# Kernel optimization log

Measured on AMD Instinct MI355X. Metric: run time of the kernel, lower is better.

The kernel has to match this reference:

```python
import jax, jax.numpy as jnp
import numpy as np
from jax import lax

LEAK = 0.01   # nn.LeakyReLU default negative slope
EPS = 1e-5    # BatchNorm2d eps


def _conv(x, w, b, stride, pad):
    # torch Conv2d, NCHW / OIHW
    y = lax.conv_general_dilated(x, w, (stride, stride), [(pad, pad), (pad, pad)],
                                 dimension_numbers=('NCHW', 'OIHW', 'NCHW'))
    return y + b[None, :, None, None]


def _bn_lrelu(x, g, b):
    # BatchNorm2d in training mode (torch default): batch statistics over (N,H,W)
    m = jnp.mean(x, axis=(0, 2, 3), keepdims=True)
    v = jnp.var(x, axis=(0, 2, 3), keepdims=True)
    xn = (x - m) * lax.rsqrt(v + EPS) * g[None, :, None, None] + b[None, :, None, None]
    return jnp.where(xn >= 0, xn, LEAK * xn)


def _convt(x, w, b):
    # ConvTranspose2d with stride == kernel_size, padding=0: non-overlapping
    # k x k expansion of every pixel -> expressible as one einsum + reshape.
    # w: (Cin, Cout, k, k) (torch ConvTranspose2d layout)
    B, C, H, W = x.shape
    _, Co, k, _ = w.shape
    y = jnp.einsum('bchw,coij->bohiwj', x, w).reshape(B, Co, H * k, W * k)
    return y + b[None, :, None, None]


def setup_inputs() -> dict:
    key = jax.random.key(0)
    ks = iter(jax.random.split(key, 64))
    def rn(shape, s=0.05):
        return jax.random.normal(next(ks), shape, dtype=jnp.float32) * s
    d = {}
    d['x'] = jax.random.normal(next(ks), (16, 3, 128, 128), dtype=jnp.float32)
    enc_shapes = [(64, 3, 4, 4), (128, 64, 4, 4), (256, 128, 4, 4), (256, 256, 4, 4)]
    for i, s in enumerate(enc_shapes):
        d[f'enc_w{i}'] = rn(s)
        d[f'enc_b{i}'] = jnp.zeros((s[0],), jnp.float32)
    for i, c in enumerate([64, 128, 256]):
        d[f'ebn_g{i}'] = jnp.ones((c,), jnp.float32)
        d[f'ebn_b{i}'] = jnp.zeros((c,), jnp.float32)
    d['codebook'] = rn((512, 256), 1.0)  # (codebook_size, latent_dim)
    dec_shapes = [(256, 128, 4, 4), (128, 64, 2, 2), (64, 32, 2, 2)]
    for i, s in enumerate(dec_shapes):
        d[f'dec_w{i}'] = rn(s)
        d[f'dec_b{i}'] = jnp.zeros((s[1],), jnp.float32)
        d[f'dbn_g{i}'] = jnp.ones((s[1],), jnp.float32)
        d[f'dbn_b{i}'] = jnp.zeros((s[1],), jnp.float32)
    d['dec_w3'] = rn((3, 32, 1, 1))
    d['dec_b3'] = jnp.zeros((3,), jnp.float32)
    return d


def reference(x,
              enc_w0, enc_b0, ebn_g0, ebn_b0,
              enc_w1, enc_b1, ebn_g1, ebn_b1,
              enc_w2, enc_b2, ebn_g2, ebn_b2,
              enc_w3, enc_b3,
              codebook,
              dec_w0, dec_b0, dbn_g0, dbn_b0,
              dec_w1, dec_b1, dbn_g1, dbn_b1,
              dec_w2, dec_b2, dbn_g2, dbn_b2,
              dec_w3, dec_b3):
    # ---- encoder ----
    h = _bn_lrelu(_conv(x, enc_w0, enc_b0, 2, 1), ebn_g0, ebn_b0)   # (B,64,64,64)
    h = _bn_lrelu(_conv(h, enc_w1, enc_b1, 2, 1), ebn_g1, ebn_b1)   # (B,128,32,32)
    h = _bn_lrelu(_conv(h, enc_w2, enc_b2, 2, 1), ebn_g2, ebn_b2)   # (B,256,16,16)
    z = _conv(h, enc_w3, enc_b3, 2, 1)                               # (B,256,8,8)

    # ---- vector quantizer ----
    B, C, H, W = z.shape
    zf = z.transpose(0, 2, 3, 1).reshape(-1, C)                      # (BHW, C)
    # squared L2 distances to every codebook entry
    d2 = (jnp.sum(zf * zf, axis=-1, keepdims=True)
          - 2.0 * zf @ codebook.T
          + jnp.sum(codebook * codebook, axis=-1)[None, :])          # (BHW, K)
    idx = jnp.argmin(d2, axis=-1)                                    # (BHW,)
    min_d = jnp.min(d2, axis=-1)
    q = codebook[idx]                                                # (BHW, C)
    commitment_loss = jnp.mean((lax.stop_gradient(q) - zf) ** 2)
    codebook_loss = jnp.mean((q - lax.stop_gradient(zf)) ** 2)
    q_st = zf + lax.stop_gradient(q - zf)                            # straight-through
    qz = q_st.reshape(B, H, W, C).transpose(0, 3, 1, 2)              # (B,256,8,8)

    # ---- decoder ----
    h = _bn_lrelu(_convt(qz, dec_w0, dec_b0), dbn_g0, dbn_b0)        # (B,128,32,32)
    h = _bn_lrelu(_convt(h, dec_w1, dec_b1), dbn_g1, dbn_b1)         # (B,64,64,64)
    h = _bn_lrelu(_convt(h, dec_w2, dec_b2), dbn_g2, dbn_b2)         # (B,32,128,128)
    out = jnp.tanh(jnp.einsum('bchw,oc->bohw', h, dec_w3[:, :, 0, 0])
                   + dec_b3[None, :, None, None])                    # (B,3,128,128)

    return (out, commitment_loss, codebook_loss,
            idx.reshape(B, H, W), min_d.reshape(B, H, W))
```

## Files before the change

kernel.cpp:

```cpp
#include <hip/hip_runtime.h>
#include <math.h>

#define LEAK 0.01f

typedef __bf16 bf16x8 __attribute__((ext_vector_type(8)));
typedef float f32x4 __attribute__((ext_vector_type(4)));
typedef unsigned short ushort;
typedef unsigned int uint32;

struct HL { ushort h, l; };

__device__ inline HL split_bf16(float x) {
    unsigned u = __float_as_uint(x);
    unsigned hr = (u + 0x7FFFu + ((u >> 16) & 1u)) >> 16;
    float fh = __uint_as_float(hr << 16);
    float r = x - fh;
    unsigned v = __float_as_uint(r);
    unsigned lr = (v + 0x7FFFu + ((v >> 16) & 1u)) >> 16;
    HL out; out.h = (ushort)hr; out.l = (ushort)lr;
    return out;
}

template<int MODE>
__device__ inline void stage_load(float (&pv)[2][4], const float* __restrict__ Bf,
                                  int kbase, int n0, int tid,
                                  int Ci, int Hin, int Ho, int lgHo, int lgHW) {
#pragma unroll
    for (int r = 0; r < 2; ++r) {
        int g = r * 256 + tid;
        int nl = g >> 3, kg = g & 7;
        int n = n0 + nl;
        if (MODE == 0) {
            int k4 = kbase + (kg << 2);
            int ic = k4 >> 4, kh = (k4 >> 2) & 3;
            int ow = n & (Ho - 1), oh = (n >> lgHo) & (Ho - 1), b = n >> (lgHo + lgHo);
            int ih = oh * 2 - 1 + kh;
            int ihc = ih < 0 ? 0 : (ih >= Hin ? Hin - 1 : ih);
            int iwb = ow * 2 - 1;
            size_t base = ((size_t)(b * Ci + ic) * Hin + ihc) * Hin;
#pragma unroll
            for (int e = 0; e < 4; ++e) {
                int iw = iwb + e;
                int iwc = iw < 0 ? 0 : (iw >= Hin ? Hin - 1 : iw);
                pv[r][e] = Bf[base + iwc];
            }
        } else {
            int c = kbase + (kg << 2);
            int b = n >> lgHW, hw = n & ((1 << lgHW) - 1);
            size_t base = (((size_t)(b * Ci + c)) << lgHW) + hw;
            size_t str = (size_t)1 << lgHW;
#pragma unroll
            for (int e = 0; e < 4; ++e) pv[r][e] = Bf[base + e * str];
        }
    }
}

template<int MODE>
__global__ __launch_bounds__(256, 3) void gemm_mfma(
    const ushort* __restrict__ Ah, const ushort* __restrict__ Al,
    const float* __restrict__ Bf,
    const float* __restrict__ bnt, const float* __restrict__ gamma,
    const float* __restrict__ beta, float invN, int chanShift,
    const float* __restrict__ bias, float* __restrict__ P,
    int Mtiles, int Ntiles, int K, int Kslice, int KS, int outSize,
    int Ci, int Hin, int Co, int Ho, int lgHo,
    int lgHW, int lgHin, int lgCo, int lgk,
    float* __restrict__ statsBnt, const float* __restrict__ bnPart)
{
    __shared__ __align__(16) uint32 Bsp[64 * 36];
    __shared__ float scs[256], shs[256];

    int bid = blockIdx.x;
    int ntile = bid % Ntiles; bid /= Ntiles;
    int mtile = bid % Mtiles;
    int ks = bid / Mtiles;
    int tid = threadIdx.x;
    int lane = tid & 63, w = tid >> 6;
    int quad = lane >> 4, tl = lane & 15;
    int n0 = ntile << 6, m0 = mtile << 7, k0 = ks * Kslice;
    int Kt = K >> 5;

    bool useBN = (bnt != nullptr) || (bnPart != nullptr);
    int c0 = k0 >> chanShift;
    if (bnPart != nullptr) {
        int c = tid >> 2, qq = tid & 3;
        const float2* pp2 = (const float2*)(bnPart + c * 512) + qq * 64;
        float s = 0.f, s2 = 0.f;
#pragma unroll 8
        for (int p = 0; p < 64; ++p) { float2 v = pp2[p]; s += v.x; s2 += v.y; }
        scs[tid] = s; shs[tid] = s2;
        __syncthreads();
        float scale = 0.f, shift = 0.f;
        if (tid < 64) {
            float st = scs[tid * 4] + scs[tid * 4 + 1] + scs[tid * 4 + 2] + scs[tid * 4 + 3];
            float qt = shs[tid * 4] + shs[tid * 4 + 1] + shs[tid * 4 + 2] + shs[tid * 4 + 3];
            float m = st * invN;
            float var = qt * invN - m * m;
            scale = gamma[tid] * rsqrtf(var + 1e-5f);
            shift = beta[tid] - m * scale;
        }
        __syncthreads();
        if (tid < 64 && tid >= c0) { scs[tid - c0] = scale; shs[tid - c0] = shift; }
    } else if (bnt != nullptr) {
        int nch = Kslice >> chanShift;
        for (int c = tid; c < nch; c += 256) {
            float m = bnt[(c0 + c) * 2] * invN;
            float var = bnt[(c0 + c) * 2 + 1] * invN - m * m;
            float scale = gamma[c0 + c] * rsqrtf(var + 1e-5f);
            scs[c] = scale;
            shs[c] = beta[c0 + c] - m * scale;
        }
    }
    __syncthreads();

    f32x4 zero4 = {0.f, 0.f, 0.f, 0.f};
    f32x4 acc[2][4];
#pragma unroll
    for (int mt = 0; mt < 2; ++mt)
#pragma unroll
        for (int nt = 0; nt < 4; ++nt) acc[mt][nt] = zero4;

    float pv[2][4];
    stage_load<MODE>(pv, Bf, k0, n0, tid, Ci, Hin, Ho, lgHo, lgHW);

    for (int kc = 0; kc < Kslice; kc += 32) {
        int kbase = k0 + kc;
        int kt = kbase >> 5;
#pragma unroll
        for (int r = 0; r < 2; ++r) {
            int g = r * 256 + tid;
            int nl = g >> 3, kg = g & 7;
            int k4 = kbase + (kg << 2);
            uint32 pk[4];
            if (MODE == 0) {
                int ic = k4 >> 4, kh = (k4 >> 2) & 3;
                int n = n0 + nl;
                int ow = n & (Ho - 1), oh = (n >> lgHo) & (Ho - 1);
                int ih = oh * 2 - 1 + kh;
                bool rowok = (unsigned)ih < (unsigned)Hin;
                int iwb = ow * 2 - 1;
                float sc_ = useBN ? scs[ic - c0] : 0.f;
                float sh_ = useBN ? shs[ic - c0] : 0.f;
#pragma unroll
                for (int e = 0; e < 4; ++e) {
                    int iw = iwb + e;
                    bool ok = rowok && ((unsigned)iw < (unsigned)Hin);
                    float f = pv[r][e];
                    if (useBN) { f = f * sc_ + sh_; f = f >= 0.f ? f : LEAK * f; }
                    if (!ok) f = 0.f;
                    HL s = split_bf16(f);
                    pk[e] = ((uint32)s.h << 16) | s.l;
                }
            } else {
#pragma unroll
                for (int e = 0; e < 4; ++e) {
                    float f = pv[r][e];
                    if (useBN) {
                        int lc = k4 + e - k0;
                        f = f * scs[lc] + shs[lc];
                        f = f >= 0.f ? f : LEAK * f;
                    }
                    HL s = split_bf16(f);
                    pk[e] = ((uint32)s.h << 16) | s.l;
                }
            }
            *(uint4*)&Bsp[nl * 36 + (kg << 2)] = make_uint4(pk[0], pk[1], pk[2], pk[3]);
        }
        __syncthreads();

        bool more = (kc + 32) < Kslice;
        float pvn[2][4];
        if (more) stage_load<MODE>(pvn, Bf, kbase + 32, n0, tid, Ci, Hin, Ho, lgHo, lgHW);

        bf16x8 afh[2], afl[2];
#pragma unroll
        for (int mt = 0; mt < 2; ++mt) {
            int mtAbs = (m0 >> 4) + (w << 1) + mt;
            size_t abase = (((size_t)mtAbs * Kt + kt) << 6) + lane;
            afh[mt] = *(const bf16x8*)(Ah + abase * 8);
            afl[mt] = *(const bf16x8*)(Al + abase * 8);
        }
        bf16x8 bfh[4], bfl[4];
#pragma unroll
        for (int nt = 0; nt < 4; ++nt) {
            int base = ((nt << 4) + tl) * 36 + (quad << 3);
            uint4 ua = *(const uint4*)&Bsp[base];
            uint4 ub = *(const uint4*)&Bsp[base + 4];
            union { uint32 u[4]; bf16x8 v; } H, L;
            H.u[0] = __builtin_amdgcn_perm(ua.y, ua.x, 0x07060302u);
            H.u[1] = __builtin_amdgcn_perm(ua.w, ua.z, 0x07060302u);
            H.u[2] = __builtin_amdgcn_perm(ub.y, ub.x, 0x07060302u);
            H.u[3] = __builtin_amdgcn_perm(ub.w, ub.z, 0x07060302u);
            L.u[0] = __builtin_amdgcn_perm(ua.y, ua.x, 0x05040100u);
            L.u[1] = __builtin_amdgcn_perm(ua.w, ua.z, 0x05040100u);
            L.u[2] = __builtin_amdgcn_perm(ub.y, ub.x, 0x05040100u);
            L.u[3] = __builtin_amdgcn_perm(ub.w, ub.z, 0x05040100u);
            bfh[nt] = H.v; bfl[nt] = L.v;
        }
#pragma unroll
        for (int mt = 0; mt < 2; ++mt)
#pragma unroll
            for (int nt = 0; nt < 4; ++nt) {
                acc[mt][nt] = __builtin_amdgcn_mfma_f32_16x16x32_bf16(afh[mt], bfh[nt], acc[mt][nt], 0, 0, 0);
                acc[mt][nt] = __builtin_amdgcn_mfma_f32_16x16x32_bf16(afh[mt], bfl[nt], acc[mt][nt], 0, 0, 0);
                acc[mt][nt] = __builtin_amdgcn_mfma_f32_16x16x32_bf16(afl[mt], bfh[nt], acc[mt][nt], 0, 0, 0);
            }
        __syncthreads();
        if (more) {
#pragma unroll
            for (int r = 0; r < 2; ++r)
#pragma unroll
                for (int e = 0; e < 4; ++e) pv[r][e] = pvn[r][e];
        }
    }

    bool doStats = (statsBnt != nullptr);
    if (doStats) {
        if (tid < 2 * Co) scs[tid] = 0.f;
        __syncthreads();
    }
    float ssum[2][4] = {{0.f,0.f,0.f,0.f},{0.f,0.f,0.f,0.f}};
    float ssq [2][4] = {{0.f,0.f,0.f,0.f},{0.f,0.f,0.f,0.f}};
    float* dst = P + (size_t)ks * outSize;
    if (MODE == 0) {
#pragma unroll
        for (int nt = 0; nt < 4; ++nt) {
            int n = n0 + (nt << 4) + tl;
            int ow = n & (Ho - 1), oh = (n >> lgHo) & (Ho - 1), b = n >> (lgHo + lgHo);
#pragma unroll
            for (int mt = 0; mt < 2; ++mt) {
                int mb = m0 + (w << 5) + (mt << 4) + (quad << 2);
#pragma unroll
                for (int r = 0; r < 4; ++r) {
                    int oc = mb + r;
                    float v = acc[mt][nt][r];
                    if (KS == 1) v += bias[oc];
                    if (doStats) { ssum[mt][r] += v; ssq[mt][r] += v * v; }
                    dst[((size_t)(b * Co + oc) * Ho + oh) * Ho + ow] = v;
                }
            }
        }
    } else {
        int kf = 1 << lgk;
        int Ho2 = Hin << lgk;
#pragma unroll
        for (int nt = 0; nt < 4; ++nt) {
            int n = n0 + (nt << 4) + tl;
            int b = n >> lgHW, hw = n & ((1 << lgHW) - 1);
            int h = hw >> lgHin, wp = hw & (Hin - 1);
#pragma unroll
            for (int mt = 0; mt < 2; ++mt) {
                int mb = m0 + (w << 5) + (mt << 4) + (quad << 2);
#pragma unroll
                for (int r = 0; r < 4; ++r) {
                    int m = mb + r;
                    int o = m & (Co - 1), ij = m >> lgCo;
                    int ii = ij >> lgk, jj = ij & (kf - 1);
                    float v = acc[mt][nt][r];
                    if (KS == 1) v += bias[o];
                    if (doStats) { ssum[mt][r] += v; ssq[mt][r] += v * v; }
                    dst[((size_t)(b * Co + o) * Ho2 + (h << lgk) + ii) * Ho2 + (wp << lgk) + jj] = v;
                }
            }
        }
    }
    if (doStats) {
#pragma unroll
        for (int mt = 0; mt < 2; ++mt)
#pragma unroll
            for (int r = 0; r < 4; ++r) {
                float s = ssum[mt][r], q2 = ssq[mt][r];
#pragma unroll
                for (int m2 = 1; m2 < 16; m2 <<= 1) {
                    s  += __shfl_xor(s,  m2);
                    q2 += __shfl_xor(q2, m2);
                }
                if (tl == 0) {
                    int m = m0 + (w << 5) + (mt << 4) + (quad << 2) + r;
                    int o = (MODE == 0) ? m : (m & (Co - 1));
                    atomicAdd(&scs[o * 2],     s);
                    atomicAdd(&scs[o * 2 + 1], q2);
                }
            }
        __syncthreads();
        if (tid < 2 * Co) atomicAdd(&statsBnt[tid], scs[tid]);
    }
}

__device__ inline int fragaddr(int m, int k, int K) {
    return ((((m >> 4) * (K >> 5) + (k >> 5)) << 9) | (((k >> 3) & 3) << 7) | ((m & 15) << 3) | (k & 7));
}

#define OUT_CL   786432
#define OUT_CB   786433
#define OUT_IDX  786434
#define OUT_MIND 787458

__device__ void conv_body(int bid, int tid,
                          const float* __restrict__ x, const float* __restrict__ w,
                          const float* __restrict__ bias, float* __restrict__ P,
                          float* __restrict__ pst, float (&cst)[4][16])
{
    const int Ci = 3, Hin = 128, Co = 64, Ho = 64, OCT = 8;
    int ntile = (16 * Ho * Ho) >> 8;
    int tile = bid % ntile;
    int og = bid / ntile;
    int oc0 = og * OCT;

    int px = (tile << 8) + tid;
    int ow = px % Ho; int t = px / Ho;
    int oh = t % Ho;  int b = t / Ho;

    int off[16]; float fm[16];
    int ih0 = oh * 2 - 1, iw0 = ow * 2 - 1;
#pragma unroll
    for (int kh = 0; kh < 4; ++kh)
#pragma unroll
        for (int kw = 0; kw < 4; ++kw) {
            int ih = ih0 + kh, iw = iw0 + kw;
            bool ok = (ih >= 0) && (ih < Hin) && (iw >= 0) && (iw < Hin);
            int ihc = ih < 0 ? 0 : (ih >= Hin ? Hin - 1 : ih);
            int iwc = iw < 0 ? 0 : (iw >= Hin ? Hin - 1 : iw);
            off[kh * 4 + kw] = ihc * Hin + iwc;
            fm[kh * 4 + kw] = ok ? 1.f : 0.f;
        }

    float acc[OCT];
#pragma unroll
    for (int u = 0; u < OCT; ++u) acc[u] = bias[oc0 + u];

    const float* xc = x + (size_t)b * Ci * Hin * Hin;
    const float* wi = w + (size_t)oc0 * Ci * 16;
    int HinHin = Hin * Hin;
    for (int ic = 0; ic < Ci; ++ic) {
        float xv[16];
#pragma unroll
        for (int q = 0; q < 16; ++q) xv[q] = xc[off[q]] * fm[q];
#pragma unroll
        for (int u = 0; u < OCT; ++u) {
            const float* wo = wi + (size_t)u * Ci * 16;
            float a = acc[u];
#pragma unroll
            for (int q = 0; q < 16; ++q) a += xv[q] * wo[q];
            acc[u] = a;
        }
        xc += HinHin;
        wi += 16;
    }
    size_t obase = (((size_t)b * Co + oc0) * Ho + oh) * Ho + ow;
    size_t opl = (size_t)Ho * Ho;
#pragma unroll
    for (int u = 0; u < OCT; ++u) P[obase + u * opl] = acc[u];

    float sv[OCT], qv[OCT];
#pragma unroll
    for (int u = 0; u < OCT; ++u) { sv[u] = acc[u]; qv[u] = acc[u] * acc[u]; }
#pragma unroll
    for (int m2 = 1; m2 < 64; m2 <<= 1)
#pragma unroll
        for (int u = 0; u < OCT; ++u) {
            sv[u] += __shfl_xor(sv[u], m2);
            qv[u] += __shfl_xor(qv[u], m2);
        }
    int lane = tid & 63, wv = tid >> 6;
    if (lane == 0) {
#pragma unroll
        for (int u = 0; u < OCT; ++u) { cst[wv][u * 2] = sv[u]; cst[wv][u * 2 + 1] = qv[u]; }
    }
    __syncthreads();
    if (tid < 2 * OCT) {
        float v = cst[0][tid] + cst[1][tid] + cst[2][tid] + cst[3][tid];
        pst[(oc0 + (tid >> 1)) * 512 + tile * 2 + (tid & 1)] = v;
    }
}

__global__ void prologue(const float* __restrict__ w1, const float* __restrict__ w2,
                         const float* __restrict__ w3, const float* __restrict__ d0,
                         const float* __restrict__ d1, const float* __restrict__ d2,
                         ushort* __restrict__ WH, ushort* __restrict__ WL,
                         const float* __restrict__ cb, float* __restrict__ cbT,
                         float* __restrict__ bnt, float* __restrict__ dout,
                         const float* __restrict__ x, const float* __restrict__ w0,
                         const float* __restrict__ b0, float* __restrict__ Y0,
                         float* __restrict__ pst) {
    __shared__ float cst[4][16];
    int blk = blockIdx.x;
    int tid = threadIdx.x;
    if (blk < 24) {
        bnt[blk * 256 + tid] = 0.f;
        if (blk == 0 && tid < 2) dout[OUT_CL + tid] = 0.f;
        return;
    }
    if (blk < 536) {
        int idx = (blk - 24) * 256 + tid;
        int k = idx & 511, c = idx >> 9;
        cbT[idx] = cb[k * 256 + c];
        return;
    }
    if (blk >= 9400) {
        conv_body(blk - 9400, tid, x, w0, b0, Y0, pst, cst);
        return;
    }
    int idx = (blk - 536) * 256 + tid;
    if (idx >= 2269184) return;
    float v; int dst;
    if (idx < 131072) {
        int m = idx >> 10, k = idx & 1023;
        v = w1[idx];
        dst = fragaddr(m, k, 1024);
    } else if (idx < 655360) {
        int i = idx - 131072;
        int m = i >> 11, k = i & 2047;
        v = w2[i];
        dst = 131072 + fragaddr(m, k, 2048);
    } else if (idx < 1703936) {
        int i = idx - 655360;
        int m = i >> 12, k = i & 4095;
        v = w3[i];
        dst = 655360 + fragaddr(m, k, 4096);
    } else if (idx < 2228224) {
        int i = idx - 1703936;
        int m = i >> 8, c = i & 255;
        int o = m & 127, ij = m >> 7;
        v = d0[((size_t)c * 128 + o) * 16 + ij];
        dst = 1703936 + fragaddr(m, c, 256);
    } else if (idx < 2260992) {
        int i = idx - 2228224;
        int m = i >> 7, c = i & 127;
        int o = m & 63, ij = m >> 6;
        v = d1[((size_t)c * 64 + o) * 4 + ij];
        dst = 2228224 + fragaddr(m, c, 128);
    } else {
        int i = idx - 2260992;
        int m = i >> 6, c = i & 63;
        int o = m & 31, ij = m >> 5;
        v = d2[((size_t)c * 32 + o) * 4 + ij];
        dst = 2260992 + fragaddr(m, c, 64);
    }
    HL s = split_bf16(v);
    WH[dst] = s.h; WL[dst] = s.l;
}

__global__ void reduce_bias_stats4(const float4* __restrict__ P, const float* __restrict__ bias,
                                   float4* __restrict__ y, float* __restrict__ bnt,
                                   int outSize4, int KS, int Co, int HW4, int nch) {
    int tid = threadIdx.x;
    int i = blockIdx.x * 256 + tid;
    int c = (i / HW4) % Co;
    float bv = bias[c];
    float4 s = make_float4(bv, bv, bv, bv);
    for (int ks = 0; ks < KS; ++ks) {
        float4 p = P[(size_t)ks * outSize4 + i];
        s.x += p.x; s.y += p.y; s.z += p.z; s.w += p.w;
    }
    y[i] = s;
    float ls  = s.x + s.y + s.z + s.w;
    float ls2 = s.x * s.x + s.y * s.y + s.z * s.z + s.w * s.w;
    __shared__ float as[16], aq[16];
    if (tid < 16) { as[tid] = 0.f; aq[tid] = 0.f; }
    __syncthreads();
    int c0 = ((blockIdx.x * 256) / HW4) % Co;
    atomicAdd(&as[c - c0], ls);
    atomicAdd(&aq[c - c0], ls2);
    __syncthreads();
    if (tid < nch) {
        atomicAdd(&bnt[(c0 + tid) * 2],     as[tid]);
        atomicAdd(&bnt[(c0 + tid) * 2 + 1], aq[tid]);
    }
}

__global__ void vq_main(const float* __restrict__ Pz, const float* __restrict__ b3,
                        const float* __restrict__ cbT, const float* __restrict__ cb,
                        float* __restrict__ q, float* __restrict__ dout) {
    int r0 = blockIdx.x * 4;
    int tid = threadIdx.x;
    int lane = tid & 63, w = tid >> 6;

    __shared__ __align__(16) float zT[256][4];
    __shared__ float wred[4][4];
    __shared__ float zn2s[4];
    __shared__ float wbd[4][4];
    __shared__ int   wbi[4][4];
    __shared__ int   bestsh[4];
    __shared__ float bestd[4];

    int b = r0 >> 6, s0 = r0 & 63;
    size_t zi = ((size_t)(b * 256 + tid)) * 64 + s0;
    float bv = b3[tid];
    float4 zv = make_float4(bv, bv, bv, bv);
    const float4* pp = (const float4*)Pz + (zi >> 2);
#pragma unroll
    for (int ks = 0; ks < 16; ++ks) {
        float4 p = pp[(size_t)ks * 65536];
        zv.x += p.x; zv.y += p.y; zv.z += p.z; zv.w += p.w;
    }
    *(float4*)&zT[tid][0] = zv;

    float p0 = zv.x * zv.x, p1 = zv.y * zv.y, p2 = zv.z * zv.z, p3 = zv.w * zv.w;
#pragma unroll
    for (int m2 = 1; m2 < 64; m2 <<= 1) {
        p0 += __shfl_xor(p0, m2); p1 += __shfl_xor(p1, m2);
        p2 += __shfl_xor(p2, m2); p3 += __shfl_xor(p3, m2);
    }
    if (lane == 0) { wred[w][0] = p0; wred[w][1] = p1; wred[w][2] = p2; wred[w][3] = p3; }
    __syncthreads();
    if (tid < 4) zn2s[tid] = wred[0][tid] + wred[1][tid] + wred[2][tid] + wred[3][tid];
    __syncthreads();

    float d0[4], d1[4];
#pragma unroll
    for (int rr = 0; rr < 4; ++rr) { d0[rr] = 0.f; d1[rr] = 0.f; }
    float cn0 = 0.f, cn1 = 0.f;
#pragma unroll 4
    for (int c = 0; c < 256; ++c) {
        float cv0 = cbT[c * 512 + tid];
        float cv1 = cbT[c * 512 + 256 + tid];
        cn0 += cv0 * cv0;
        cn1 += cv1 * cv1;
        float4 za = *(const float4*)&zT[c][0];
        d0[0] += za.x * cv0; d1[0] += za.x * cv1;
        d0[1] += za.y * cv0; d1[1] += za.y * cv1;
        d0[2] += za.z * cv0; d1[2] += za.z * cv1;
        d0[3] += za.w * cv0; d1[3] += za.w * cv1;
    }

#pragma unroll
    for (int rr = 0; rr < 4; ++rr) {
        float dist0 = zn2s[rr] - 2.f * d0[rr] + cn0;
        float dist1 = zn2s[rr] - 2.f * d1[rr] + cn1;
        float bd = dist0; int bi = tid;
        if (dist1 < bd) { bd = dist1; bi = tid + 256; }
#pragma unroll
        for (int m2 = 1; m2 < 64; m2 <<= 1) {
            float od = __shfl_xor(bd, m2); int oi = __shfl_xor(bi, m2);
            if (od < bd || (od == bd && oi < bi)) { bd = od; bi = oi; }
        }
        if (lane == 0) { wbd[w][rr] = bd; wbi[w][rr] = bi; }
    }
    __syncthreads();
    if (tid < 4) {
        float bd = wbd[0][tid]; int bi = wbi[0][tid];
#pragma unroll
        for (int ww = 1; ww < 4; ++ww) {
            float od = wbd[ww][tid]; int oi = wbi[ww][tid];
            if (od < bd || (od == bd && oi < bi)) { bd = od; bi = oi; }
        }
        bestsh[tid] = bi; bestd[tid] = bd;
        dout[OUT_IDX + r0 + tid]  = (float)bi;
        dout[OUT_MIND + r0 + tid] = bd;
    }
    __syncthreads();

    float4 qv;
    qv.x = cb[(size_t)bestsh[0] * 256 + tid];
    qv.y = cb[(size_t)bestsh[1] * 256 + tid];
    qv.z = cb[(size_t)bestsh[2] * 256 + tid];
    qv.w = cb[(size_t)bestsh[3] * 256 + tid];
    *(float4*)&q[((size_t)(b * 256 + tid)) * 64 + s0] = qv;
    if (tid == 0) {
        float ls = (bestd[0] + bestd[1] + bestd[2] + bestd[3]) * (1.f / 262144.f);
        atomicAdd(&dout[OUT_CL], ls);
        atomicAdd(&dout[OUT_CB], ls);
    }
}

__global__ void final_conv_tanh(const float* __restrict__ hbuf, const float* __restrict__ bnt,
                                const float* __restrict__ g, const float* __restrict__ bt,
                                const float* __restrict__ w3, const float* __restrict__ b3,
                                float* __restrict__ out) {
    __shared__ float sc[32], sh[32], sw[96];
    int tid = threadIdx.x;
    if (tid < 32) {
        float m = bnt[tid * 2] * (1.f / 262144.f);
        float var = bnt[tid * 2 + 1] * (1.f / 262144.f) - m * m;
        float scale = g[tid] * rsqrtf(var + 1e-5f);
        sc[tid] = scale;
        sh[tid] = bt[tid] - m * scale;
    }
    if (tid < 96) sw[tid] = w3[tid];
    __syncthreads();
    int idx = blockIdx.x * 256 + tid;
    int hw4 = idx & 4095;
    int b   = idx >> 12;
    const float4* hp = (const float4*)hbuf + ((size_t)b * 32) * 4096 + hw4;
    float b0 = b3[0], b1 = b3[1], b2 = b3[2];
    float4 a0 = make_float4(b0, b0, b0, b0);
    float4 a1 = make_float4(b1, b1, b1, b1);
    float4 a2 = make_float4(b2, b2, b2, b2);
#pragma unroll 8
    for (int c = 0; c < 32; ++c) {
        float4 v = hp[(size_t)c * 4096];
        float scv = sc[c], shv = sh[c];
        float vx = v.x * scv + shv; vx = vx >= 0.f ? vx : LEAK * vx;
        float vy = v.y * scv + shv; vy = vy >= 0.f ? vy : LEAK * vy;
        float vz = v.z * scv + shv; vz = vz >= 0.f ? vz : LEAK * vz;
        float vw = v.w * scv + shv; vw = vw >= 0.f ? vw : LEAK * vw;
        float w0 = sw[c], w1 = sw[32 + c], w2 = sw[64 + c];
        a0.x += vx * w0; a0.y += vy * w0; a0.z += vz * w0; a0.w += vw * w0;
        a1.x += vx * w1; a1.y += vy * w1; a1.z += vz * w1; a1.w += vw * w1;
        a2.x += vx * w2; a2.y += vy * w2; a2.z += vz * w2; a2.w += vw * w2;
    }
    float4* op = (float4*)out;
    size_t ob = ((size_t)b * 3) * 4096 + hw4;
    op[ob]            = make_float4(tanhf(a0.x), tanhf(a0.y), tanhf(a0.z), tanhf(a0.w));
    op[ob + 4096]     = make_float4(tanhf(a1.x), tanhf(a1.y), tanhf(a1.z), tanhf(a1.w));
    op[ob + 2 * 4096] = make_float4(tanhf(a2.x), tanhf(a2.y), tanhf(a2.z), tanhf(a2.w));
}

extern "C" void kernel_launch(void* const* d_in, const int* in_sizes, int n_in,
                              void* d_out, int out_size, void* d_ws, size_t ws_size,
                              hipStream_t stream) {
    const float* x      = (const float*)d_in[0];
    const float* enc_w0 = (const float*)d_in[1];
    const float* enc_b0 = (const float*)d_in[2];
    const float* enc_w1 = (const float*)d_in[3];
    const float* enc_b1 = (const float*)d_in[4];
    const float* enc_w2 = (const float*)d_in[5];
    const float* enc_b2 = (const float*)d_in[6];
    const float* enc_w3 = (const float*)d_in[7];
    const float* enc_b3 = (const float*)d_in[8];
    const float* ebn_g0 = (const float*)d_in[9];
    const float* ebn_b0 = (const float*)d_in[10];
    const float* ebn_g1 = (const float*)d_in[11];
    const float* ebn_b1 = (const float*)d_in[12];
    const float* ebn_g2 = (const float*)d_in[13];
    const float* ebn_b2 = (const float*)d_in[14];
    const float* cb     = (const float*)d_in[15];
    const float* dec_w0 = (const float*)d_in[16];
    const float* dec_b0 = (const float*)d_in[17];
    const float* dbn_g0 = (const float*)d_in[18];
    const float* dbn_b0 = (const float*)d_in[19];
    const float* dec_w1 = (const float*)d_in[20];
    const float* dec_b1 = (const float*)d_in[21];
    const float* dbn_g1 = (const float*)d_in[22];
    const float* dbn_b1 = (const float*)d_in[23];
    const float* dec_w2 = (const float*)d_in[24];
    const float* dec_b2 = (const float*)d_in[25];
    const float* dbn_g2 = (const float*)d_in[26];
    const float* dbn_b2 = (const float*)d_in[27];
    const float* dec_w3 = (const float*)d_in[28];
    const float* dec_b3 = (const float*)d_in[29];

    float* out = (float*)d_out;
    float* ws  = (float*)d_ws;

    float*  Y0   = ws;
    float*  Y1   = ws + 4194304;
    float*  Y2   = ws + 6291456;
    float*  PST  = ws + 7340032;
    float*  Q    = ws + 7602176;
    ushort* WH   = (ushort*)(ws + 7864320);
    ushort* WL   = (ushort*)(ws + 8998912);
    float*  CBT  = ws + 10133504;
    float*  BNT  = ws + 10264576;
    float*  PART = ws + 10270720;
    float*  D0   = ws + 18659328;
    float*  D1   = ws + 20756480;
    float*  D2   = ws + 24950784;

    dim3 blk(256);

    prologue<<<11448, blk, 0, stream>>>(enc_w1, enc_w2, enc_w3, dec_w0, dec_w1, dec_w2,
                                        WH, WL, cb, CBT, BNT, out,
                                        x, enc_w0, enc_b0, Y0, PST);

    gemm_mfma<0><<<512, blk, 0, stream>>>(WH, WL, Y0,
        nullptr, ebn_g0, ebn_b0, 1.f / 65536.f, 4, enc_b1, PART,
        1, 256, 1024, 512, 2, 2097152, 64, 64, 128, 32, 5, 0, 0, 0, 0, nullptr, PST);
    reduce_bias_stats4<<<2048, blk, 0, stream>>>((const float4*)PART, enc_b1, (float4*)Y1,
                                                 BNT + 1024, 524288, 2, 128, 256, 1);

    gemm_mfma<0><<<512, blk, 0, stream>>>(WH + 131072, WL + 131072, Y1,
        BNT + 1024, ebn_g1, ebn_b1, 1.f / 16384.f, 4, enc_b2, PART,
        2, 64, 2048, 512, 4, 1048576, 128, 32, 256, 16, 4, 0, 0, 0, 0, nullptr, nullptr);
    reduce_bias_stats4<<<1024, blk, 0, stream>>>((const float4*)PART, enc_b2, (float4*)Y2,
                                                 BNT + 2048, 262144, 4, 256, 64, 4);

    gemm_mfma<0><<<512, blk, 0, stream>>>(WH + 655360, WL + 655360, Y2,
        BNT + 2048, ebn_g2, ebn_b2, 1.f / 4096.f, 4, enc_b3, PART,
        2, 16, 4096, 256, 16, 262144, 256, 16, 256, 8, 3, 0, 0, 0, 0, nullptr, nullptr);

    vq_main<<<256, blk, 0, stream>>>(PART, enc_b3, CBT, cb, Q, out);

    gemm_mfma<1><<<512, blk, 0, stream>>>(WH + 1703936, WL + 1703936, Q,
        nullptr, nullptr, nullptr, 0.f, 0, dec_b0, PART,
        16, 16, 256, 128, 2, 2097152, 256, 8, 128, 0, 0, 6, 3, 7, 2, nullptr, nullptr);
    reduce_bias_stats4<<<2048, blk, 0, stream>>>((const float4*)PART, dec_b0, (float4*)D0,
                                                 BNT + 3072, 524288, 2, 128, 256, 1);

    gemm_mfma<1><<<512, blk, 0, stream>>>(WH + 2228224, WL + 2228224, D0,
        BNT + 3072, dbn_g0, dbn_b0, 1.f / 16384.f, 0, dec_b1, D1,
        2, 256, 128, 128, 1, 0, 128, 32, 64, 0, 0, 10, 5, 6, 1, BNT + 4096, nullptr);

    gemm_mfma<1><<<1024, blk, 0, stream>>>(WH + 2260992, WL + 2260992, D1,
        BNT + 4096, dbn_g1, dbn_b1, 1.f / 65536.f, 0, dec_b2, D2,
        1, 1024, 64, 64, 1, 0, 64, 64, 32, 0, 0, 12, 6, 5, 1, BNT + 5120, nullptr);

    final_conv_tanh<<<256, blk, 0, stream>>>(D2, BNT + 5120, dbn_g2, dbn_b2, dec_w3, dec_b3, out);
}
```

Measured before the change: 416.9 us.

## Emit pre-split bf16 quantized latents and bank BN stat atomics across eight slots

The VQ kernel now writes the quantized vectors as pre-split bf16 hi/lo arrays in row-major (pixel, channel) layout. A new GEMM mode 2 loads these directly as MFMA B fragments from global memory, skipping LDS staging, the split conversion and the block barriers for the first decoder layer. Separately, per-block BN statistic atomics are spread over eight banks indexed by block id, and consumers sum the banks, to reduce atomic contention. The risks are that direct global fragment loads may coalesce poorly, and that the bank buffers need zero-initialisation that is not shown here.

```diff
diff --git a/kernel.cpp b/kernel.cpp
--- a/kernel.cpp
+++ b/kernel.cpp
@@ -65,7 +65,8 @@
     int Mtiles, int Ntiles, int K, int Kslice, int KS, int outSize,
     int Ci, int Hin, int Co, int Ho, int lgHo,
     int lgHW, int lgHin, int lgCo, int lgk,
-    float* __restrict__ statsBnt, const float* __restrict__ bnPart)
+    float* __restrict__ statsBnt, const float* __restrict__ bnPart,
+    int statsBank, int bntBankStride)
 {
     __shared__ __align__(16) uint32 Bsp[64 * 36];
     __shared__ float scs[256], shs[256];
@@ -104,8 +105,20 @@
     } else if (bnt != nullptr) {
         int nch = Kslice >> chanShift;
         for (int c = tid; c < nch; c += 256) {
-            float m = bnt[(c0 + c) * 2] * invN;
-            float var = bnt[(c0 + c) * 2 + 1] * invN - m * m;
+            float sm, sq;
+            if (bntBankStride > 0) {
+                sm = 0.f; sq = 0.f;
+#pragma unroll
+                for (int bk = 0; bk < 8; ++bk) {
+                    sm += bnt[bk * bntBankStride + (c0 + c) * 2];
+                    sq += bnt[bk * bntBankStride + (c0 + c) * 2 + 1];
+                }
+            } else {
+                sm = bnt[(c0 + c) * 2];
+                sq = bnt[(c0 + c) * 2 + 1];
+            }
+            float m = sm * invN;
+            float var = sq * invN - m * m;
             float scale = gamma[c0 + c] * rsqrtf(var + 1e-5f);
             scs[c] = scale;
             shs[c] = beta[c0 + c] - m * scale;
@@ -121,56 +134,58 @@
         for (int nt = 0; nt < 4; ++nt) acc[mt][nt] = zero4;
 
     float pv[2][4];
-    stage_load<MODE>(pv, Bf, k0, n0, tid, Ci, Hin, Ho, lgHo, lgHW);
+    if (MODE != 2) stage_load<MODE>(pv, Bf, k0, n0, tid, Ci, Hin, Ho, lgHo, lgHW);
 
     for (int kc = 0; kc < Kslice; kc += 32) {
         int kbase = k0 + kc;
         int kt = kbase >> 5;
-#pragma unroll
-        for (int r = 0; r < 2; ++r) {
-            int g = r * 256 + tid;
-            int nl = g >> 3, kg = g & 7;
-            int k4 = kbase + (kg << 2);
-            uint32 pk[4];
-            if (MODE == 0) {
-                int ic = k4 >> 4, kh = (k4 >> 2) & 3;
-                int n = n0 + nl;
-                int ow = n & (Ho - 1), oh = (n >> lgHo) & (Ho - 1);
-                int ih = oh * 2 - 1 + kh;
-                bool rowok = (unsigned)ih < (unsigned)Hin;
-                int iwb = ow * 2 - 1;
-                float sc_ = useBN ? scs[ic - c0] : 0.f;
-                float sh_ = useBN ? shs[ic - c0] : 0.f;
-#pragma unroll
-                for (int e = 0; e < 4; ++e) {
-                    int iw = iwb + e;
-                    bool ok = rowok && ((unsigned)iw < (unsigned)Hin);
-                    float f = pv[r][e];
-                    if (useBN) { f = f * sc_ + sh_; f = f >= 0.f ? f : LEAK * f; }
-                    if (!ok) f = 0.f;
-                    HL s = split_bf16(f);
-                    pk[e] = ((uint32)s.h << 16) | s.l;
-                }
-            } else {
-#pragma unroll
-                for (int e = 0; e < 4; ++e) {
-                    float f = pv[r][e];
-                    if (useBN) {
-                        int lc = k4 + e - k0;
-                        f = f * scs[lc] + shs[lc];
-                        f = f >= 0.f ? f : LEAK * f;
-                    }
-                    HL s = split_bf16(f);
-                    pk[e] = ((uint32)s.h << 16) | s.l;
-                }
-            }
-            *(uint4*)&Bsp[nl * 36 + (kg << 2)] = make_uint4(pk[0], pk[1], pk[2], pk[3]);
-        }
-        __syncthreads();
-
         bool more = (kc + 32) < Kslice;
         float pvn[2][4];
-        if (more) stage_load<MODE>(pvn, Bf, kbase + 32, n0, tid, Ci, Hin, Ho, lgHo, lgHW);
+        if (MODE != 2) {
+#pragma unroll
+            for (int r = 0; r < 2; ++r) {
+                int g = r * 256 + tid;
+                int nl = g >> 3, kg = g & 7;
+                int k4 = kbase + (kg << 2);
+                uint32 pk[4];
+                if (MODE == 0) {
+                    int ic = k4 >> 4, kh = (k4 >> 2) & 3;
+                    int n = n0 + nl;
+                    int ow = n & (Ho - 1), oh = (n >> lgHo) & (Ho - 1);
+                    int ih = oh * 2 - 1 + kh;
+                    bool rowok = (unsigned)ih < (unsigned)Hin;
+                    int iwb = ow * 2 - 1;
+                    float sc_ = useBN ? scs[ic - c0] : 0.f;
+                    float sh_ = useBN ? shs[ic - c0] : 0.f;
+#pragma unroll
+                    for (int e = 0; e < 4; ++e) {
+                        int iw = iwb + e;
+                        bool ok = rowok && ((unsigned)iw < (unsigned)Hin);
+                        float f = pv[r][e];
+                        if (useBN) { f = f * sc_ + sh_; f = f >= 0.f ? f : LEAK * f; }
+                        if (!ok) f = 0.f;
+                        HL s = split_bf16(f);
+                        pk[e] = ((uint32)s.h << 16) | s.l;
+                    }
+                } else {
+#pragma unroll
+                    for (int e = 0; e < 4; ++e) {
+                        float f = pv[r][e];
+                        if (useBN) {
+                            int lc = k4 + e - k0;
+                            f = f * scs[lc] + shs[lc];
+                            f = f >= 0.f ? f : LEAK * f;
+                        }
+                        HL s = split_bf16(f);
+                        pk[e] = ((uint32)s.h << 16) | s.l;
+                    }
+                }
+                *(uint4*)&Bsp[nl * 36 + (kg << 2)] = make_uint4(pk[0], pk[1], pk[2], pk[3]);
+            }
+            __syncthreads();
+
+            if (more) stage_load<MODE>(pvn, Bf, kbase + 32, n0, tid, Ci, Hin, Ho, lgHo, lgHW);
+        }
 
         bf16x8 afh[2], afl[2];
 #pragma unroll
@@ -181,21 +196,32 @@
             afl[mt] = *(const bf16x8*)(Al + abase * 8);
         }
         bf16x8 bfh[4], bfl[4];
-#pragma unroll
-        for (int nt = 0; nt < 4; ++nt) {
-            int base = ((nt << 4) + tl) * 36 + (quad << 3);
-            uint4 ua = *(const uint4*)&Bsp[base];
-            uint4 ub = *(const uint4*)&Bsp[base + 4];
-            union { uint32 u[4]; bf16x8 v; } H, L;
-            H.u[0] = __builtin_amdgcn_perm(ua.y, ua.x, 0x07060302u);
-            H.u[1] = __builtin_amdgcn_perm(ua.w, ua.z, 0x07060302u);
-            H.u[2] = __builtin_amdgcn_perm(ub.y, ub.x, 0x07060302u);
-            H.u[3] = __builtin_amdgcn_perm(ub.w, ub.z, 0x07060302u);
-            L.u[0] = __builtin_amdgcn_perm(ua.y, ua.x, 0x05040100u);
-            L.u[1] = __builtin_amdgcn_perm(ua.w, ua.z, 0x05040100u);
-            L.u[2] = __builtin_amdgcn_perm(ub.y, ub.x, 0x05040100u);
-            L.u[3] = __builtin_amdgcn_perm(ub.w, ub.z, 0x05040100u);
-            bfh[nt] = H.v; bfl[nt] = L.v;
+        if (MODE == 2) {
+            const ushort* Bu = (const ushort*)Bf;
+#pragma unroll
+            for (int nt = 0; nt < 4; ++nt) {
+                int n = n0 + (nt << 4) + tl;
+                size_t ba = (size_t)n * Ci + kbase + (quad << 3);
+                bfh[nt] = *(const bf16x8*)(Bu + ba);
+                bfl[nt] = *(const bf16x8*)(Bu + Ho + ba);
+            }
+        } else {
+#pragma unroll
+            for (int nt = 0; nt < 4; ++nt) {
+                int base = ((nt << 4) + tl) * 36 + (quad << 3);
+                uint4 ua = *(const uint4*)&Bsp[base];
+                uint4 ub = *(const uint4*)&Bsp[base + 4];
+                union { uint32 u[4]; bf16x8 v; } H, L;
+                H.u[0] = __builtin_amdgcn_perm(ua.y, ua.x, 0x07060302u);
+                H.u[1] = __builtin_amdgcn_perm(ua.w, ua.z, 0x07060302u);
+                H.u[2] = __builtin_amdgcn_perm(ub.y, ub.x, 0x07060302u);
+                H.u[3] = __builtin_amdgcn_perm(ub.w, ub.z, 0x07060302u);
+                L.u[0] = __builtin_amdgcn_perm(ua.y, ua.x, 0x05040100u);
+                L.u[1] = __builtin_amdgcn_perm(ua.w, ua.z, 0x05040100u);
+                L.u[2] = __builtin_amdgcn_perm(ub.y, ub.x, 0x05040100u);
+                L.u[3] = __builtin_amdgcn_perm(ub.w, ub.z, 0x05040100u);
+                bfh[nt] = H.v; bfl[nt] = L.v;
+            }
         }
 #pragma unroll
         for (int mt = 0; mt < 2; ++mt)
@@ -205,12 +231,14 @@
                 acc[mt][nt] = __builtin_amdgcn_mfma_f32_16x16x32_bf16(afh[mt], bfl[nt], acc[mt][nt], 0, 0, 0);
                 acc[mt][nt] = __builtin_amdgcn_mfma_f32_16x16x32_bf16(afl[mt], bfh[nt], acc[mt][nt], 0, 0, 0);
             }
-        __syncthreads();
-        if (more) {
-#pragma unroll
-            for (int r = 0; r < 2; ++r)
-#pragma unroll
-                for (int e = 0; e < 4; ++e) pv[r][e] = pvn[r][e];
+        if (MODE != 2) {
+            __syncthreads();
+            if (more) {
+#pragma unroll
+                for (int r = 0; r < 2; ++r)
+#pragma unroll
+                    for (int e = 0; e < 4; ++e) pv[r][e] = pvn[r][e];
+            }
         }
     }
 
@@ -283,7 +311,8 @@
                 }
             }
         __syncthreads();
-        if (tid < 2 * Co) atomicAdd(&statsBnt[tid], scs[tid]);
+        float* sb = statsBnt + (blockIdx.x & 7) * statsBank;
+        if (tid < 2 * Co) atomicAdd(&sb[tid], scs[tid]);
     }
 }
 
@@ -471,7 +500,7 @@
 
 __global__ void vq_main(const float* __restrict__ Pz, const float* __restrict__ b3,
                         const float* __restrict__ cbT, const float* __restrict__ cb,
-                        float* __restrict__ q, float* __restrict__ dout) {
+                        ushort* __restrict__ qhl, float* __restrict__ dout) {
     int r0 = blockIdx.x * 4;
     int tid = threadIdx.x;
     int lane = tid & 63, w = tid >> 6;
@@ -551,12 +580,14 @@
     }
     __syncthreads();
 
-    float4 qv;
-    qv.x = cb[(size_t)bestsh[0] * 256 + tid];
-    qv.y = cb[(size_t)bestsh[1] * 256 + tid];
-    qv.z = cb[(size_t)bestsh[2] * 256 + tid];
-    qv.w = cb[(size_t)bestsh[3] * 256 + tid];
-    *(float4*)&q[((size_t)(b * 256 + tid)) * 64 + s0] = qv;
+#pragma unroll
+    for (int rr = 0; rr < 4; ++rr) {
+        float v = cb[(size_t)bestsh[rr] * 256 + tid];
+        HL s = split_bf16(v);
+        size_t o = (size_t)(r0 + rr) * 256 + tid;
+        qhl[o]          = s.h;
+        qhl[262144 + o] = s.l;
+    }
     if (tid == 0) {
         float ls = (bestd[0] + bestd[1] + bestd[2] + bestd[3]) * (1.f / 262144.f);
         atomicAdd(&dout[OUT_CL], ls);
@@ -571,8 +602,14 @@
     __shared__ float sc[32], sh[32], sw[96];
     int tid = threadIdx.x;
     if (tid < 32) {
-        float m = bnt[tid * 2] * (1.f / 262144.f);
-        float var = bnt[tid * 2 + 1] * (1.f / 262144.f) - m * m;
+        float sm = 0.f, sq = 0.f;
+#pragma unroll
+        for (int bk = 0; bk < 8; ++bk) {
+            sm += bnt[bk * 64 + tid * 2];
+            sq += bnt[bk * 64 + tid * 2 + 1];
+        }
+        float m = sm * (1.f / 262144.f);
+        float var = sq * (1.f / 262144.f) - m * m;
         float scale = g[tid] * rsqrtf(var + 1e-5f);
         sc[tid] = scale;
         sh[tid] = bt[tid] - m * scale;
@@ -648,7 +685,7 @@
     float*  Y1   = ws + 4194304;
     float*  Y2   = ws + 6291456;
     float*  PST  = ws + 7340032;
-    float*  Q    = ws + 7602176;
+    float*  QHL  = ws + 7602176;
     ushort* WH   = (ushort*)(ws + 7864320);
     ushort* WL   = (ushort*)(ws + 8998912);
     float*  CBT  = ws + 10133504;
@@ -666,35 +703,35 @@
 
     gemm_mfma<0><<<512, blk, 0, stream>>>(WH, WL, Y0,
         nullptr, ebn_g0, ebn_b0, 1.f / 65536.f, 4, enc_b1, PART,
-        1, 256, 1024, 512, 2, 2097152, 64, 64, 128, 32, 5, 0, 0, 0, 0, nullptr, PST);
+        1, 256, 1024, 512, 2, 2097152, 64, 64, 128, 32, 5, 0, 0, 0, 0, nullptr, PST, 0, 0);
     reduce_bias_stats4<<<2048, blk, 0, stream>>>((const float4*)PART, enc_b1, (float4*)Y1,
                                                  BNT + 1024, 524288, 2, 128, 256, 1);
 
     gemm_mfma<0><<<512, blk, 0, stream>>>(WH + 131072, WL + 131072, Y1,
         BNT + 1024, ebn_g1, ebn_b1, 1.f / 16384.f, 4, enc_b2, PART,
-        2, 64, 2048, 512, 4, 1048576, 128, 32, 256, 16, 4, 0, 0, 0, 0, nullptr, nullptr);
+        2, 64, 2048, 512, 4, 1048576, 128, 32, 256, 16, 4, 0, 0, 0, 0, nullptr, nullptr, 0, 0);
     reduce_bias_stats4<<<1024, blk, 0, stream>>>((const float4*)PART, enc_b2, (float4*)Y2,
                                                  BNT + 2048, 262144, 4, 256, 64, 4);
 
     gemm_mfma<0><<<512, blk, 0, stream>>>(WH + 655360, WL + 655360, Y2,
         BNT + 2048, ebn_g2, ebn_b2, 1.f / 4096.f, 4, enc_b3, PART,
-        2, 16, 4096, 256, 16, 262144, 256, 16, 256, 8, 3, 0, 0, 0, 0, nullptr, nullptr);
-
-    vq_main<<<256, blk, 0, stream>>>(PART, enc_b3, CBT, cb, Q, out);
-
-    gemm_mfma<1><<<512, blk, 0, stream>>>(WH + 1703936, WL + 1703936, Q,
+        2, 16, 4096, 256, 16, 262144, 256, 16, 256, 8, 3, 0, 0, 0, 0, nullptr, nullptr, 0, 0);
+
+    vq_main<<<256, blk, 0, stream>>>(PART, enc_b3, CBT, cb, (ushort*)QHL, out);
+
+    gemm_mfma<2><<<512, blk, 0, stream>>>(WH + 1703936, WL + 1703936, QHL,
         nullptr, nullptr, nullptr, 0.f, 0, dec_b0, PART,
-        16, 16, 256, 128, 2, 2097152, 256, 8, 128, 0, 0, 6, 3, 7, 2, nullptr, nullptr);
+        16, 16, 256, 128, 2, 2097152, 256, 8, 128, 262144, 0, 6, 3, 7, 2, nullptr, nullptr, 0, 0);
     reduce_bias_stats4<<<2048, blk, 0, stream>>>((const float4*)PART, dec_b0, (float4*)D0,
                                                  BNT + 3072, 524288, 2, 128, 256, 1);
 
     gemm_mfma<1><<<512, blk, 0, stream>>>(WH + 2228224, WL + 2228224, D0,
         BNT + 3072, dbn_g0, dbn_b0, 1.f / 16384.f, 0, dec_b1, D1,
-        2, 256, 128, 128, 1, 0, 128, 32, 64, 0, 0, 10, 5, 6, 1, BNT + 4096, nullptr);
+        2, 256, 128, 128, 1, 0, 128, 32, 64, 0, 0, 10, 5, 6, 1, BNT + 4096, nullptr, 128, 0);
 
     gemm_mfma<1><<<1024, blk, 0, stream>>>(WH + 2260992, WL + 2260992, D1,
         BNT + 4096, dbn_g1, dbn_b1, 1.f / 65536.f, 0, dec_b2, D2,
-        1, 1024, 64, 64, 1, 0, 64, 64, 32, 0, 0, 12, 6, 5, 1, BNT + 5120, nullptr);
+        1, 1024, 64, 64, 1, 0, 64, 64, 32, 0, 0, 12, 6, 5, 1, BNT + 5120, nullptr, 64, 128);
 
     final_conv_tanh<<<256, blk, 0, stream>>>(D2, BNT + 5120, dbn_g2, dbn_b2, dec_w3, dec_b3, out);
 }
```

Result: faster. 388.3 us (-6.8%).
